# Kernel tuning notes

Hardware: AMD Instinct MI355X
Metric: run time of the kernel (lower is better)

The kernel has to match this reference:

```python
import jax, jax.numpy as jnp
import numpy as np
from math import ceil

SCALE = (0.25, 0.25)
IM_SIZE = (1080, 1920)
KERNEL_WIDTH = 4.0


def _cubic(x):
    absx = np.abs(x)
    absx2 = absx * absx
    absx3 = absx2 * absx
    return ((1.5 * absx3 - 2.5 * absx2 + 1) * (absx <= 1)
            + (-0.5 * absx3 + 2.5 * absx2 - 4 * absx + 2) * ((1 < absx) * (absx <= 2)))


def _contributions(in_length, out_length, scale):
    # MATLAB-style imresize contributions (matches the torch module's numpy code)
    if scale < 1:
        h = lambda v: scale * _cubic(scale * v)
        kernel_width = KERNEL_WIDTH / scale
    else:
        h = _cubic
        kernel_width = KERNEL_WIDTH
    x = np.arange(1, out_length + 1).astype(np.float64)
    u = x / scale + 0.5 * (1 - 1 / scale)
    left = np.floor(u - kernel_width / 2)
    P = int(ceil(kernel_width)) + 2
    ind = np.expand_dims(left, axis=1) + np.arange(P) - 1
    indices = ind.astype(np.int32)
    weights = h(np.expand_dims(u, axis=1) - indices - 1)
    weights = weights / np.sum(weights, axis=1, keepdims=True)
    aux = np.concatenate((np.arange(in_length), np.arange(in_length - 1, -1, -1))).astype(np.int32)
    indices = aux[np.mod(indices, aux.size)]
    keep = np.nonzero(np.any(weights, axis=0))[0]
    return weights[:, keep].astype(np.float32), indices[:, keep].astype(np.int64)


def setup_inputs() -> dict:
    key = jax.random.key(0)
    B, C = 8, 3
    H, W = IM_SIZE
    x = jax.random.normal(key, (B, C, H, W), dtype=jnp.float32)
    out_h = int(ceil(SCALE[0] * H))
    out_w = int(ceil(SCALE[1] * W))
    w_h, idx_h = _contributions(H, out_h, SCALE[0])
    w_w, idx_w = _contributions(W, out_w, SCALE[1])
    return {
        "x": x,
        "w_h": jnp.asarray(w_h), "idx_h": jnp.asarray(idx_h),
        "w_w": jnp.asarray(w_w), "idx_w": jnp.asarray(idx_w),
    }


def reference(x, w_h, idx_h, w_w, idx_w):
    # x: [B, C, H, W] -> work in [B, H, W, C] like the torch transpose dance
    xb = jnp.transpose(x, (0, 2, 3, 1))
    # scale is equal along both axes -> argsort order is [0, 1]: resize H then W
    # gather rows: [B, outH, P, W, C], contract over P with weights [outH, P]
    g = xb[:, idx_h, :, :]
    xb = jnp.einsum("op,bopwc->bowc", w_h, g)
    # gather cols: [B, outH, outW, P, C]
    g = xb[:, :, idx_w, :]
    xb = jnp.einsum("op,bhopc->bhoc", w_w, g)
    return jnp.transpose(xb, (0, 3, 1, 2))
```

## Files before the change

kernel.cpp:

```cpp
#include <hip/hip_runtime.h>

namespace {

constexpr int H  = 1080;
constexpr int W  = 1920;
constexpr int OH = 270;
constexpr int OW = 480;
constexpr int KT = 16;
constexpr int G  = 14;
constexpr int NCH = 19;

__global__ __launch_bounds__(256) void bicubic_main(
    const float* __restrict__ x,
    const float* __restrict__ wh,
    const float* __restrict__ ww,
    float*       __restrict__ out)
{
    const int ow = blockIdx.x * blockDim.x + threadIdx.x;
    if (ow < 2 || ow > OW - 3) return;
    const int oh0 = 2 + blockIdx.y * G;
    const int bc  = blockIdx.z;

    float wt[KT];
    __builtin_memcpy(wt, ww + (size_t)ow * KT, KT * sizeof(float));

    float wr[KT];
    __builtin_memcpy(wr, wh + (size_t)oh0 * KT, KT * sizeof(float));

    const int i0 = 4 * ow  - 6;
    const int r0 = 4 * oh0 - 6;
    const float* __restrict__ base =
        x + (size_t)bc * ((size_t)H * W) + (size_t)r0 * W + i0;
    float* __restrict__ obase =
        out + ((size_t)bc * OH) * OW + ow;

    float a0 = 0.f, a1 = 0.f, a2 = 0.f, a3 = 0.f;

    for (int j = 0; j < G + 3; ++j) {
        float h[4];
        #pragma unroll
        for (int p = 0; p < 4; ++p) {
            float v[KT];
            __builtin_memcpy(v, base + (size_t)(4 * j + p) * W,
                             KT * sizeof(float));
            float s0 = 0.f, s1 = 0.f;
            #pragma unroll
            for (int k = 0; k < KT; k += 2) {
                s0 = fmaf(v[k],     wt[k],     s0);
                s1 = fmaf(v[k + 1], wt[k + 1], s1);
            }
            h[p] = s0 + s1;
        }
        #pragma unroll
        for (int p = 0; p < 4; ++p) {
            a0 = fmaf(wr[p],      h[p], a0);
            a1 = fmaf(wr[4 + p],  h[p], a1);
            a2 = fmaf(wr[8 + p],  h[p], a2);
            a3 = fmaf(wr[12 + p], h[p], a3);
        }
        if (j >= 3) obase[(size_t)(oh0 + j - 3) * OW] = a3;
        a3 = a2; a2 = a1; a1 = a0; a0 = 0.f;
    }
}

constexpr int EDGE_FULL = 4 * OW;
constexpr int EDGE_TOT  = EDGE_FULL + (OH - 4) * 4;

__global__ __launch_bounds__(256) void bicubic_edge(
    const float* __restrict__ x,
    const float* __restrict__ wh,
    const int*   __restrict__ ih,
    const float* __restrict__ ww,
    const int*   __restrict__ iw,
    float*       __restrict__ out)
{
    const int idx = blockIdx.x * blockDim.x + threadIdx.x;
    const int bc  = blockIdx.y;
    if (idx >= EDGE_TOT) return;

    int oh, ow;
    if (idx < EDGE_FULL) {
        int e = idx / OW;
        ow = idx - e * OW;
        oh = (e < 2) ? e : OH - 4 + e;
    } else {
        int t = idx - EDGE_FULL;
        int e = t & 3;
        oh = 2 + (t >> 2);
        ow = (e < 2) ? e : OW - 4 + e;
    }

    const float* __restrict__ img = x + (size_t)bc * ((size_t)H * W);

    float wt[KT];
    __builtin_memcpy(wt, ww + (size_t)ow * KT, KT * sizeof(float));
    int ir[KT];
    __builtin_memcpy(ir, iw + (size_t)ow * KT, KT * sizeof(int));

    bool fast = true;
    #pragma unroll
    for (int k = 1; k < KT; ++k) fast = fast && (ir[k] == ir[0] + k);
    const int i0 = ir[0];

    float acc = 0.0f;
    #pragma unroll 4
    for (int kh = 0; kh < KT; ++kh) {
        const int   r = ih[oh * KT + kh];
        const float w = wh[oh * KT + kh];
        const float* row = img + (size_t)r * W;
        float h = 0.0f;
        if (fast) {
            float v[KT];
            __builtin_memcpy(v, row + i0, KT * sizeof(float));
            #pragma unroll
            for (int k = 0; k < KT; ++k) h = fmaf(v[k], wt[k], h);
        } else {
            #pragma unroll
            for (int k = 0; k < KT; ++k) h = fmaf(row[ir[k]], wt[k], h);
        }
        acc = fmaf(w, h, acc);
    }
    out[((size_t)bc * OH + oh) * OW + ow] = acc;
}

__global__ __launch_bounds__(256) void bicubic_generic(
    const float* __restrict__ x,
    const float* __restrict__ wh,
    const int*   __restrict__ ih,
    const float* __restrict__ ww,
    const int*   __restrict__ iw,
    float*       __restrict__ out,
    int Kh, int Kw, int total)
{
    int t = blockIdx.x * blockDim.x + threadIdx.x;
    if (t >= total) return;
    int ow = t % OW;
    int oh = (t / OW) % OH;
    int bc = t / (OW * OH);
    const float* img = x + (size_t)bc * ((size_t)H * W);
    float acc = 0.0f;
    for (int kh = 0; kh < Kh; ++kh) {
        const int   r = ih[oh * Kh + kh];
        const float w = wh[oh * Kh + kh];
        const float* row = img + (size_t)r * W;
        float h = 0.0f;
        for (int k = 0; k < Kw; ++k)
            h = fmaf(row[iw[ow * Kw + k]], ww[ow * Kw + k], h);
        acc = fmaf(w, h, acc);
    }
    out[t] = acc;
}

}

extern "C" void kernel_launch(void* const* d_in, const int* in_sizes, int n_in,
                              void* d_out, int out_size, void* d_ws, size_t ws_size,
                              hipStream_t stream) {
    const float* x  = (const float*)d_in[0];
    const float* wh = (const float*)d_in[1];
    const int*   ih = (const int*)d_in[2];
    const float* ww = (const float*)d_in[3];
    const int*   iw = (const int*)d_in[4];
    float*       out = (float*)d_out;

    const int BC = in_sizes[0] / (H * W);
    const int Kh = in_sizes[1] / OH;
    const int Kw = in_sizes[3] / OW;

    if (Kh == KT && Kw == KT) {
        dim3 mg((OW + 255) / 256, NCH, BC);
        bicubic_main<<<mg, 256, 0, stream>>>(x, wh, ww, out);
        dim3 eg((EDGE_TOT + 255) / 256, BC, 1);
        bicubic_edge<<<eg, 256, 0, stream>>>(x, wh, ih, ww, iw, out);
    } else {
        int total = BC * OH * OW;
        bicubic_generic<<<(total + 255) / 256, 256, 0, stream>>>(
            x, wh, ih, ww, iw, out, Kh, Kw, total);
    }
}
```

Before: 341.1 us.

## Split separable resize into vertical pass to LDS then horizontal pass

```diff
diff --git a/kernel.cpp b/kernel.cpp
--- a/kernel.cpp
+++ b/kernel.cpp
@@ -7,59 +7,86 @@
 constexpr int OH = 270;
 constexpr int OW = 480;
 constexpr int KT = 16;
-constexpr int G  = 14;
-constexpr int NCH = 19;
-
-__global__ __launch_bounds__(256) void bicubic_main(
+constexpr int G  = 7;
+constexpr int NCHUNK = 38;
+constexpr int COLS = 1024;
+constexpr int VSTRIDE = 1028;
+
+__global__ __launch_bounds__(256) void bicubic_tile(
     const float* __restrict__ x,
     const float* __restrict__ wh,
     const float* __restrict__ ww,
     float*       __restrict__ out)
 {
-    const int ow = blockIdx.x * blockDim.x + threadIdx.x;
-    if (ow < 2 || ow > OW - 3) return;
-    const int oh0 = 2 + blockIdx.y * G;
-    const int bc  = blockIdx.z;
-
-    float wt[KT];
-    __builtin_memcpy(wt, ww + (size_t)ow * KT, KT * sizeof(float));
+    __shared__ float vbuf[G * VSTRIDE];
+
+    const int tid  = threadIdx.x;
+    const int tile = blockIdx.x;
+    const int oh0  = 2 + G * blockIdx.y;
+    const int bc   = blockIdx.z;
+
+    const int ow_base = (tile == 0) ? 2   : 255;
+    const int Nw      = (tile == 0) ? 253 : 223;
+    const int c0      = 4 * ow_base - 6;
+    const int r0      = 4 * oh0 - 6;
 
     float wr[KT];
-    __builtin_memcpy(wr, wh + (size_t)oh0 * KT, KT * sizeof(float));
-
-    const int i0 = 4 * ow  - 6;
-    const int r0 = 4 * oh0 - 6;
-    const float* __restrict__ base =
-        x + (size_t)bc * ((size_t)H * W) + (size_t)r0 * W + i0;
-    float* __restrict__ obase =
-        out + ((size_t)bc * OH) * OW + ow;
-
-    float a0 = 0.f, a1 = 0.f, a2 = 0.f, a3 = 0.f;
-
-    for (int j = 0; j < G + 3; ++j) {
-        float h[4];
+    __builtin_memcpy(wr, wh + (size_t)oh0 * KT, sizeof(wr));
+
+    int c = c0 + 4 * tid;
+    if (c > W - 4) c = W - 4;
+    const float* __restrict__ col = x + ((size_t)bc * H + (size_t)r0) * W + c;
+
+    float acc[4][4];
+    #pragma unroll
+    for (int m = 0; m < 4; ++m)
+        #pragma unroll
+        for (int cc = 0; cc < 4; ++cc) acc[m][cc] = 0.0f;
+
+    for (int q = 0; q < G + 3; ++q) {
         #pragma unroll
         for (int p = 0; p < 4; ++p) {
+            float v[4];
+            __builtin_memcpy(v, col + (size_t)(4 * q + p) * W, 16);
+            #pragma unroll
+            for (int cc = 0; cc < 4; ++cc) {
+                acc[0][cc] = fmaf(wr[p],      v[cc], acc[0][cc]);
+                acc[1][cc] = fmaf(wr[4 + p],  v[cc], acc[1][cc]);
+                acc[2][cc] = fmaf(wr[8 + p],  v[cc], acc[2][cc]);
+                acc[3][cc] = fmaf(wr[12 + p], v[cc], acc[3][cc]);
+            }
+        }
+        if (q >= 3) {
+            __builtin_memcpy(&vbuf[(q - 3) * VSTRIDE + 4 * tid], acc[3], 16);
+        }
+        #pragma unroll
+        for (int cc = 0; cc < 4; ++cc) {
+            acc[3][cc] = acc[2][cc];
+            acc[2][cc] = acc[1][cc];
+            acc[1][cc] = acc[0][cc];
+            acc[0][cc] = 0.0f;
+        }
+    }
+    __syncthreads();
+
+    if (tid < Nw) {
+        const int ow = ow_base + tid;
+        float wt[KT];
+        __builtin_memcpy(wt, ww + (size_t)ow * KT, sizeof(wt));
+        float* __restrict__ obase =
+            out + ((size_t)bc * OH + oh0) * OW + ow;
+        #pragma unroll
+        for (int t = 0; t < G; ++t) {
             float v[KT];
-            __builtin_memcpy(v, base + (size_t)(4 * j + p) * W,
-                             KT * sizeof(float));
+            __builtin_memcpy(v, &vbuf[t * VSTRIDE + 4 * tid], sizeof(v));
             float s0 = 0.f, s1 = 0.f;
             #pragma unroll
             for (int k = 0; k < KT; k += 2) {
                 s0 = fmaf(v[k],     wt[k],     s0);
                 s1 = fmaf(v[k + 1], wt[k + 1], s1);
             }
-            h[p] = s0 + s1;
-        }
-        #pragma unroll
-        for (int p = 0; p < 4; ++p) {
-            a0 = fmaf(wr[p],      h[p], a0);
-            a1 = fmaf(wr[4 + p],  h[p], a1);
-            a2 = fmaf(wr[8 + p],  h[p], a2);
-            a3 = fmaf(wr[12 + p], h[p], a3);
-        }
-        if (j >= 3) obase[(size_t)(oh0 + j - 3) * OW] = a3;
-        a3 = a2; a2 = a1; a1 = a0; a0 = 0.f;
+            obase[(size_t)t * OW] = s0 + s1;
+        }
     }
 }
 
@@ -93,9 +120,9 @@
     const float* __restrict__ img = x + (size_t)bc * ((size_t)H * W);
 
     float wt[KT];
-    __builtin_memcpy(wt, ww + (size_t)ow * KT, KT * sizeof(float));
+    __builtin_memcpy(wt, ww + (size_t)ow * KT, sizeof(wt));
     int ir[KT];
-    __builtin_memcpy(ir, iw + (size_t)ow * KT, KT * sizeof(int));
+    __builtin_memcpy(ir, iw + (size_t)ow * KT, sizeof(ir));
 
     bool fast = true;
     #pragma unroll
@@ -111,7 +138,7 @@
         float h = 0.0f;
         if (fast) {
             float v[KT];
-            __builtin_memcpy(v, row + i0, KT * sizeof(float));
+            __builtin_memcpy(v, row + i0, sizeof(v));
             #pragma unroll
             for (int k = 0; k < KT; ++k) h = fmaf(v[k], wt[k], h);
         } else {
@@ -168,8 +195,8 @@
     const int Kw = in_sizes[3] / OW;
 
     if (Kh == KT && Kw == KT) {
-        dim3 mg((OW + 255) / 256, NCH, BC);
-        bicubic_main<<<mg, 256, 0, stream>>>(x, wh, ww, out);
+        dim3 mg(2, NCHUNK, BC);
+        bicubic_tile<<<mg, 256, 0, stream>>>(x, wh, ww, out);
         dim3 eg((EDGE_TOT + 255) / 256, BC, 1);
         bicubic_edge<<<eg, 256, 0, stream>>>(x, wh, ih, ww, iw, out);
     } else {
```

After: 325.4 us. 1.05x faster.
